# Kernel tuning notes

Hardware: AMD Instinct MI355X
Metric: run time of the kernel (lower is better)

The kernel has to match this reference:

```python
import jax, jax.numpy as jnp
import numpy as np

N, E, H, ED = 20000, 320000, 256, 64  # nodes, edges, hidden_dim, edge_feature_dim


def setup_inputs() -> dict:
    key = jax.random.key(0)
    ks = jax.random.split(key, 12)

    def init_w(k, shape, fan_in):
        return (jax.random.normal(k, shape, jnp.float32) / np.sqrt(fan_in)).astype(jnp.float32)

    h = jax.random.normal(ks[0], (N, H), jnp.float32)
    edge_indices = jax.random.randint(ks[1], (2, E), 0, N, jnp.int32)
    edge_attr = jax.random.normal(ks[2], (E, ED), jnp.float32)

    din = 2 * H + ED  # edge_network input: [h[row], h[col], edge_attr]
    W1 = init_w(ks[3], (H, din), din)
    b1 = jnp.zeros((H,), jnp.float32)
    W2 = init_w(ks[4], (H, H), H)
    b2 = jnp.zeros((H,), jnp.float32)
    # GRUCell params, gate order (r, z, n) as in torch
    W_ih = init_w(ks[5], (3 * H, H), H)
    b_ih = jnp.zeros((3 * H,), jnp.float32)
    W_hh = init_w(ks[6], (3 * H, H), H)
    b_hh = jnp.zeros((3 * H,), jnp.float32)

    return {"h": h, "edge_indices": edge_indices, "edge_attr": edge_attr,
            "W1": W1, "b1": b1, "W2": W2, "b2": b2,
            "W_ih": W_ih, "b_ih": b_ih, "W_hh": W_hh, "b_hh": b_hh}


def reference(h, edge_indices, edge_attr, W1, b1, W2, b2, W_ih, b_ih, W_hh, b_hh):
    row, col = edge_indices[0], edge_indices[1]
    # message: edge_network MLP on [h[row], h[col], edge_attr]
    edge_in = jnp.concatenate([h[row], h[col], edge_attr], axis=-1)  # [E, 2H+ED]
    msg = jax.nn.relu(edge_in @ W1.T + b1) @ W2.T + b2               # [E, H]
    # scatter_add aggregation by destination node (row)
    agg = jax.ops.segment_sum(msg, row, num_segments=h.shape[0])     # [N, H]
    # GRUCell update: input=agg, hidden=h
    gx = agg @ W_ih.T + b_ih
    gh = h @ W_hh.T + b_hh
    xr, xz, xn = jnp.split(gx, 3, axis=-1)
    hr, hz, hn = jnp.split(gh, 3, axis=-1)
    r = jax.nn.sigmoid(xr + hr)
    z = jax.nn.sigmoid(xz + hz)
    n = jnp.tanh(xn + r * hn)
    h_new = (1.0 - z) * n + z * h
    return h_new  # dropout p=0.0 -> identity
```

## Files before the change

kernel.cpp:

```cpp
#include <hip/hip_runtime.h>
#include <math.h>

#define NN 20000
#define NE 320000
#define HD 256
#define EDIM 64
#define DIN 576
#define ASTRIDE 264

typedef __attribute__((ext_vector_type(4))) _Float16 h4;
typedef __attribute__((ext_vector_type(8))) _Float16 h8;
typedef __attribute__((ext_vector_type(4))) float f32x4;

__device__ _Float16 g_W1cf[16 * 2 * 64 * 8];
__device__ _Float16 g_W12f[32 * 8 * 64 * 8];
__device__ _Float16 g_Wrzf[32 * 16 * 64 * 8];
__device__ _Float16 g_Wnxf[16 * 8 * 64 * 8];
__device__ _Float16 g_Wnhf[16 * 8 * 64 * 8];
__device__ float    g_Wib2[768];
__device__ _Float16 g_pre[(size_t)NN * 512];
__device__ _Float16 g_hf[(size_t)NN * 256];
__device__ _Float16 g_S16[(size_t)NN * 256];
__device__ _Float16 g_msg[(size_t)NE * 256];
__device__ int      g_rowptr[NN + 1];
__device__ int      g_cursor[NN];

__device__ __forceinline__ h4 f2h4(float4 v) {
  return (h4){(_Float16)v.x, (_Float16)v.y, (_Float16)v.z, (_Float16)v.w};
}
__device__ __forceinline__ h8 f2h8(float4 a, float4 b) {
  return (h8){(_Float16)a.x, (_Float16)a.y, (_Float16)a.z, (_Float16)a.w,
              (_Float16)b.x, (_Float16)b.y, (_Float16)b.z, (_Float16)b.w};
}

__global__ __launch_bounds__(256) void cvtfold_kernel(
    const float* __restrict__ W1, const float* __restrict__ W_hh,
    const float* __restrict__ W_ih, const float* __restrict__ W2,
    const float* __restrict__ b2)
{
  const int bid = blockIdx.x;
  if (bid < 768) {
    const int r = bid, c = threadIdx.x;
    const float* wr = W_ih + (size_t)r * HD;
    float acc = 0.f;
    for (int m = 0; m < HD; ++m) acc += wr[m] * W2[(size_t)m * HD + c];
    const int ks = c >> 5, lg = (c >> 3) & 3, j = c & 7;
    const int l = lg * 16 + (r & 15);
    if (r < 512) {
      const int cf = (r < 256) ? (r >> 4) : (16 + ((r - 256) >> 4));
      g_Wrzf[(size_t)((cf * 16 + ks) * 64 + l) * 8 + j] = (_Float16)acc;
    } else {
      const int cf = (r - 512) >> 4;
      g_Wnxf[(size_t)((cf * 8 + ks) * 64 + l) * 8 + j] = (_Float16)acc;
    }
    if (c == 0) {
      float a2 = 0.f;
      for (int m = 0; m < HD; ++m) a2 += wr[m] * b2[m];
      g_Wib2[r] = a2;
    }
    return;
  }
  const int idx = (bid - 768) * 256 + threadIdx.x;
  const int g = idx >> 6, l = idx & 63;
  const int r16 = l & 15, koff = (l >> 4) * 8;
  const float* src; _Float16* dst;
  if (g < 32) {
    const int cf = g >> 1, ks = g & 1;
    src = &W1[(size_t)(cf * 16 + r16) * DIN + 512 + ks * 32 + koff];
    dst = &g_W1cf[(size_t)(cf * 2 + ks) * 512 + l * 8];
  } else if (g < 288) {
    const int gg = g - 32, cf = gg >> 3, ks = gg & 7;
    src = (cf < 16) ? &W1[(size_t)(cf * 16 + r16) * DIN + ks * 32 + koff]
                    : &W1[(size_t)((cf - 16) * 16 + r16) * DIN + 256 + ks * 32 + koff];
    dst = &g_W12f[(size_t)(cf * 8 + ks) * 512 + l * 8];
  } else if (g < 544) {
    const int gg = g - 288, cf = gg >> 3, ks = 8 + (gg & 7);
    const int row = (cf < 16) ? cf * 16 + r16 : 256 + (cf - 16) * 16 + r16;
    src = &W_hh[(size_t)row * HD + (ks - 8) * 32 + koff];
    dst = &g_Wrzf[(size_t)(cf * 16 + ks) * 512 + l * 8];
  } else {
    const int gg = g - 544, cf = gg >> 3, ks = gg & 7;
    src = &W_hh[(size_t)(512 + cf * 16 + r16) * HD + ks * 32 + koff];
    dst = &g_Wnhf[(size_t)(cf * 8 + ks) * 512 + l * 8];
  }
#pragma unroll
  for (int j = 0; j < 8; ++j) dst[j] = (_Float16)src[j];
}

#define PSTR 264
__global__ __launch_bounds__(256, 4) void pre_kernel(const float* __restrict__ h,
                                                     const int* __restrict__ ei,
                                                     int* __restrict__ deg) {
  __shared__ _Float16 A[32 * PSTR];
  const int t = threadIdx.x, w = t >> 6, l = t & 63;
  const int l15 = l & 15, lg = l >> 4;
  const int nb = blockIdx.x * 32;

  {
    const int gid = blockIdx.x * 256 + t;
    atomicAdd(&deg[ei[gid]], 1);
    atomicAdd(&deg[ei[gid + NE / 2]], 1);
  }

  const int row = t >> 3, c8 = t & 7;
#pragma unroll
  for (int i = 0; i < 8; ++i) {
    const int col4 = c8 + i * 8;
    float4 v = ((const float4*)(h + (size_t)(nb + row) * HD))[col4];
    const h4 x = f2h4(v);
    *(h4*)&A[row * PSTR + col4 * 4] = x;
    *(h4*)&g_hf[(size_t)(nb + row) * 256 + col4 * 4] = x;
  }
  __syncthreads();

  f32x4 acc[2][8];
#pragma unroll
  for (int m = 0; m < 2; ++m)
#pragma unroll
    for (int n = 0; n < 8; ++n) acc[m][n] = (f32x4){0.f, 0.f, 0.f, 0.f};

  for (int ks = 0; ks < 8; ++ks) {
    h8 a[2];
#pragma unroll
    for (int m = 0; m < 2; ++m)
      a[m] = *(const h8*)&A[(m * 16 + l15) * PSTR + ks * 32 + lg * 8];
#pragma unroll
    for (int n = 0; n < 8; ++n) {
      const h8 b = *(const h8*)&g_W12f[(size_t)((w * 8 + n) * 8 + ks) * 512 + l * 8];
#pragma unroll
      for (int m = 0; m < 2; ++m)
        acc[m][n] = __builtin_amdgcn_mfma_f32_16x16x32_f16(a[m], b, acc[m][n], 0, 0, 0);
    }
  }

#pragma unroll
  for (int m = 0; m < 2; ++m)
#pragma unroll
    for (int n = 0; n < 8; ++n) {
      const int col = w * 128 + n * 16 + l15;
#pragma unroll
      for (int r = 0; r < 4; ++r)
        g_pre[(size_t)(nb + m * 16 + lg * 4 + r) * 512 + col] = (_Float16)acc[m][n][r];
    }
}

__global__ __launch_bounds__(512) void scan_kernel(const int* __restrict__ deg) {
  __shared__ int part[512];
  const int t = threadIdx.x;
  const int base = t * 40;
  int loc[40];
  int s = 0;
#pragma unroll
  for (int i = 0; i < 40; ++i) {
    const int idx = base + i;
    const int d = (idx < NN) ? deg[idx] : 0;
    loc[i] = s; s += d;
  }
  part[t] = s;
  __syncthreads();
  for (int off = 1; off < 512; off <<= 1) {
    const int v = (t >= off) ? part[t - off] : 0;
    __syncthreads();
    part[t] += v;
    __syncthreads();
  }
  const int pre = (t == 0) ? 0 : part[t - 1];
#pragma unroll
  for (int i = 0; i < 40; ++i) {
    const int idx = base + i;
    if (idx < NN) { const int v = pre + loc[i]; g_rowptr[idx] = v; g_cursor[idx] = v; }
  }
  if (t == 511) g_rowptr[NN] = part[511];
}

__global__ __launch_bounds__(256, 4) void msg_kernel(const float* __restrict__ eattr,
                                                     const int* __restrict__ ei) {
  __shared__ _Float16 T[64 * ASTRIDE];
  __shared__ int pL[64];
  const int t = threadIdx.x, w = t >> 6, l = t & 63;
  const int l15 = l & 15, lg = l >> 4;
  const int e0 = blockIdx.x * 64;

  if (t < 64) pL[t] = atomicAdd(&g_cursor[ei[e0 + t]], 1);

  h4 q2[16];
#pragma unroll
  for (int i = 0; i < 16; ++i) {
    const int srcn = ei[NE + e0 + w * 16 + i];
    q2[i] = *(const h4*)&g_pre[(size_t)srcn * 512 + 256 + l * 4];
  }

  f32x4 acc[4][4];
#pragma unroll
  for (int m = 0; m < 4; ++m)
#pragma unroll
    for (int n = 0; n < 4; ++n) acc[m][n] = (f32x4){0.f, 0.f, 0.f, 0.f};

#pragma unroll
  for (int ks = 0; ks < 2; ++ks) {
    h8 a[4], b[4];
#pragma unroll
    for (int m = 0; m < 4; ++m) {
      const float* ep = eattr + (size_t)(e0 + m * 16 + l15) * EDIM + ks * 32 + lg * 8;
      a[m] = f2h8(((const float4*)ep)[0], ((const float4*)ep)[1]);
    }
#pragma unroll
    for (int n = 0; n < 4; ++n)
      b[n] = *(const h8*)&g_W1cf[(size_t)((w * 4 + n) * 2 + ks) * 512 + l * 8];
#pragma unroll
    for (int m = 0; m < 4; ++m)
#pragma unroll
      for (int n = 0; n < 4; ++n)
        acc[m][n] = __builtin_amdgcn_mfma_f32_16x16x32_f16(a[m], b[n], acc[m][n], 0, 0, 0);
  }

#pragma unroll
  for (int m = 0; m < 4; ++m)
#pragma unroll
    for (int n = 0; n < 4; ++n)
#pragma unroll
      for (int r = 0; r < 4; ++r)
        T[(m * 16 + lg * 4 + r) * ASTRIDE + w * 64 + n * 16 + l15] = (_Float16)acc[m][n][r];
  __syncthreads();

#pragma unroll
  for (int i = 0; i < 16; ++i) {
    const int e = w * 16 + i;
    const h4 tt = *(const h4*)&T[e * ASTRIDE + l * 4];
    h4 o;
#pragma unroll
    for (int r = 0; r < 4; ++r)
      o[r] = (_Float16)((float)tt[r] + (float)q2[i][r]);
    *(h4*)&g_msg[(size_t)pL[e] * 256 + l * 4] = o;
  }
}

__global__ __launch_bounds__(256) void agg_kernel(const float* __restrict__ b1) {
  const int t = threadIdx.x, w = t >> 6, l = t & 63;
  const int n = blockIdx.x * 4 + w;
  const int start = g_rowptr[n];
  const int end = g_rowptr[n + 1];

  const h4 p1 = *(const h4*)&g_pre[(size_t)n * 512 + l * 4];
  const f32x4 b1v = *(const f32x4*)&b1[l * 4];
  f32x4 base;
#pragma unroll
  for (int r = 0; r < 4; ++r) base[r] = (float)p1[r] + b1v[r];

  f32x4 acc = (f32x4){0.f, 0.f, 0.f, 0.f};
  int p = start;
  for (; p + 4 <= end; p += 4) {
    h4 m[4];
#pragma unroll
    for (int k = 0; k < 4; ++k)
      m[k] = *(const h4*)&g_msg[(size_t)(p + k) * 256 + l * 4];
#pragma unroll
    for (int k = 0; k < 4; ++k)
#pragma unroll
      for (int r = 0; r < 4; ++r) {
        const float v = base[r] + (float)m[k][r];
        acc[r] += v > 0.f ? v : 0.f;
      }
  }
  for (; p < end; ++p) {
    const h4 m0 = *(const h4*)&g_msg[(size_t)p * 256 + l * 4];
#pragma unroll
    for (int r = 0; r < 4; ++r) {
      const float v = base[r] + (float)m0[r];
      acc[r] += v > 0.f ? v : 0.f;
    }
  }
  *(h4*)&g_S16[(size_t)n * 256 + l * 4] =
      (h4){(_Float16)acc[0], (_Float16)acc[1], (_Float16)acc[2], (_Float16)acc[3]};
}

__global__ __launch_bounds__(256, 2) void node_kernel(
    const float* __restrict__ b_ih, const float* __restrict__ b_hh,
    float* __restrict__ out)
{
  const int bid = blockIdx.x;
  const int cf = bid & 3, rng = bid >> 2;
  const int t = threadIdx.x, w = t >> 6, l = t & 63;
  const int l15 = l & 15, lg = l >> 4;
  const int nb = rng * 64;
  const int cf0 = cf * 4;
  int na = nb + w * 16 + l15; if (na >= NN) na = NN - 1;

  f32x4 ar[4], az[4], ax[4], ah[4];
#pragma unroll
  for (int n = 0; n < 4; ++n) {
    ar[n] = (f32x4){0.f, 0.f, 0.f, 0.f}; az[n] = (f32x4){0.f, 0.f, 0.f, 0.f};
    ax[n] = (f32x4){0.f, 0.f, 0.f, 0.f}; ah[n] = (f32x4){0.f, 0.f, 0.f, 0.f};
  }

  const _Float16* aS = &g_S16[(size_t)na * 256 + lg * 8];
  const _Float16* aH = &g_hf[(size_t)na * 256 + lg * 8];

#pragma unroll
  for (int ks = 0; ks < 8; ++ks) {
    const h8 a = *(const h8*)&aS[ks * 32];
    h8 br[4], bz[4], bn[4];
#pragma unroll
    for (int n = 0; n < 4; ++n) {
      br[n] = *(const h8*)&g_Wrzf[(size_t)(((cf0 + n) * 16 + ks) * 64 + l) * 8];
      bz[n] = *(const h8*)&g_Wrzf[(size_t)(((16 + cf0 + n) * 16 + ks) * 64 + l) * 8];
      bn[n] = *(const h8*)&g_Wnxf[(size_t)(((cf0 + n) * 8 + ks) * 64 + l) * 8];
    }
#pragma unroll
    for (int n = 0; n < 4; ++n) {
      ar[n] = __builtin_amdgcn_mfma_f32_16x16x32_f16(a, br[n], ar[n], 0, 0, 0);
      az[n] = __builtin_amdgcn_mfma_f32_16x16x32_f16(a, bz[n], az[n], 0, 0, 0);
      ax[n] = __builtin_amdgcn_mfma_f32_16x16x32_f16(a, bn[n], ax[n], 0, 0, 0);
    }
  }

#pragma unroll
  for (int ks = 0; ks < 8; ++ks) {
    const h8 a = *(const h8*)&aH[ks * 32];
    h8 br[4], bz[4], bn[4];
#pragma unroll
    for (int n = 0; n < 4; ++n) {
      br[n] = *(const h8*)&g_Wrzf[(size_t)(((cf0 + n) * 16 + 8 + ks) * 64 + l) * 8];
      bz[n] = *(const h8*)&g_Wrzf[(size_t)(((16 + cf0 + n) * 16 + 8 + ks) * 64 + l) * 8];
      bn[n] = *(const h8*)&g_Wnhf[(size_t)(((cf0 + n) * 8 + ks) * 64 + l) * 8];
    }
#pragma unroll
    for (int n = 0; n < 4; ++n) {
      ar[n] = __builtin_amdgcn_mfma_f32_16x16x32_f16(a, br[n], ar[n], 0, 0, 0);
      az[n] = __builtin_amdgcn_mfma_f32_16x16x32_f16(a, bz[n], az[n], 0, 0, 0);
      ah[n] = __builtin_amdgcn_mfma_f32_16x16x32_f16(a, bn[n], ah[n], 0, 0, 0);
    }
  }

#pragma unroll
  for (int r = 0; r < 4; ++r) {
    const int node = nb + w * 16 + lg * 4 + r;
    if (node >= NN) continue;
    const float df = (float)(g_rowptr[node + 1] - g_rowptr[node]);
#pragma unroll
    for (int n = 0; n < 4; ++n) {
      const int c = cf * 64 + n * 16 + l15;
      const float rg = 1.f / (1.f + __expf(-(ar[n][r] + df * g_Wib2[c] + b_ih[c] + b_hh[c])));
      const float zg = 1.f / (1.f + __expf(-(az[n][r] + df * g_Wib2[HD + c] + b_ih[HD + c] + b_hh[HD + c])));
      const float u  = ax[n][r] + df * g_Wib2[2 * HD + c] + b_ih[2 * HD + c]
                       + rg * (ah[n][r] + b_hh[2 * HD + c]);
      const float eu = __expf(2.f * fabsf(u));
      const float ng = copysignf(1.f - 2.f / (eu + 1.f), u);
      const float hv = (float)g_hf[(size_t)node * 256 + c];
      out[(size_t)node * HD + c] = (1.f - zg) * ng + zg * hv;
    }
  }
}

extern "C" void kernel_launch(void* const* d_in, const int* in_sizes, int n_in,
                              void* d_out, int out_size, void* d_ws, size_t ws_size,
                              hipStream_t stream)
{
  const float* h     = (const float*)d_in[0];
  const int*   ei    = (const int*)d_in[1];
  const float* eattr = (const float*)d_in[2];
  const float* W1    = (const float*)d_in[3];
  const float* b1    = (const float*)d_in[4];
  const float* W2    = (const float*)d_in[5];
  const float* b2    = (const float*)d_in[6];
  const float* W_ih  = (const float*)d_in[7];
  const float* b_ih  = (const float*)d_in[8];
  const float* W_hh  = (const float*)d_in[9];
  const float* b_hh  = (const float*)d_in[10];
  float* out = (float*)d_out;

  int* deg = (int*)d_ws;

  hipMemsetAsync(deg, 0, (size_t)NN * 4, stream);
  cvtfold_kernel<<<768 + 168, 256, 0, stream>>>(W1, W_hh, W_ih, W2, b2);
  pre_kernel<<<NN / 32, 256, 0, stream>>>(h, ei, deg);
  scan_kernel<<<1, 512, 0, stream>>>(deg);
  msg_kernel<<<NE / 64, 256, 0, stream>>>(eattr, ei);
  agg_kernel<<<NN / 4, 256, 0, stream>>>(b1);
  node_kernel<<<1252, 256, 0, stream>>>(b_ih, b_hh, out);
}
```

Measured before the change: 324.2 us.

## Sort edges by source node so message gathers of source projections are local

Adds source-degree counting and a second scan, plus a new permutation kernel that orders edges by source node. That kernel stores fp16 edge attributes in source order along with a link to each edge's destination-sorted slot. The message kernel then processes edges in source order, so the gathers of precomputed source projections hit repeated or nearby rows and reuse cache, and its scattered writes go to destination-ordered positions. The cost is an extra kernel launch, extra atomics, and an extra pass that writes and re-reads the edge attributes and index arrays.

```diff
diff --git a/kernel.cpp b/kernel.cpp
--- a/kernel.cpp
+++ b/kernel.cpp
@@ -21,9 +21,13 @@
 __device__ _Float16 g_pre[(size_t)NN * 512];
 __device__ _Float16 g_hf[(size_t)NN * 256];
 __device__ _Float16 g_S16[(size_t)NN * 256];
+__device__ _Float16 g_ea16[(size_t)NE * EDIM];
 __device__ _Float16 g_msg[(size_t)NE * 256];
 __device__ int      g_rowptr[NN + 1];
-__device__ int      g_cursor[NN];
+__device__ int      g_cursor_d[NN];
+__device__ int      g_cursor_s[NN];
+__device__ int      g_ssrc[NE];
+__device__ int      g_link[NE];
 
 __device__ __forceinline__ h4 f2h4(float4 v) {
   return (h4){(_Float16)v.x, (_Float16)v.y, (_Float16)v.z, (_Float16)v.w};
@@ -90,7 +94,8 @@
 #define PSTR 264
 __global__ __launch_bounds__(256, 4) void pre_kernel(const float* __restrict__ h,
                                                      const int* __restrict__ ei,
-                                                     int* __restrict__ deg) {
+                                                     int* __restrict__ deg_d,
+                                                     int* __restrict__ deg_s) {
   __shared__ _Float16 A[32 * PSTR];
   const int t = threadIdx.x, w = t >> 6, l = t & 63;
   const int l15 = l & 15, lg = l >> 4;
@@ -98,8 +103,10 @@
 
   {
     const int gid = blockIdx.x * 256 + t;
-    atomicAdd(&deg[ei[gid]], 1);
-    atomicAdd(&deg[ei[gid + NE / 2]], 1);
+    atomicAdd(&deg_d[ei[gid]], 1);
+    atomicAdd(&deg_d[ei[gid + NE / 2]], 1);
+    atomicAdd(&deg_s[ei[NE + gid]], 1);
+    atomicAdd(&deg_s[ei[NE + gid + NE / 2]], 1);
   }
 
   const int row = t >> 3, c8 = t & 7;
@@ -144,9 +151,12 @@
     }
 }
 
-__global__ __launch_bounds__(512) void scan_kernel(const int* __restrict__ deg) {
+__global__ __launch_bounds__(512) void scan_kernel(const int* __restrict__ deg_d,
+                                                   const int* __restrict__ deg_s) {
   __shared__ int part[512];
   const int t = threadIdx.x;
+  const int isD = blockIdx.x == 0;
+  const int* deg = isD ? deg_d : deg_s;
   const int base = t * 40;
   int loc[40];
   int s = 0;
@@ -168,27 +178,46 @@
 #pragma unroll
   for (int i = 0; i < 40; ++i) {
     const int idx = base + i;
-    if (idx < NN) { const int v = pre + loc[i]; g_rowptr[idx] = v; g_cursor[idx] = v; }
-  }
-  if (t == 511) g_rowptr[NN] = part[511];
-}
-
-__global__ __launch_bounds__(256, 4) void msg_kernel(const float* __restrict__ eattr,
-                                                     const int* __restrict__ ei) {
-  __shared__ _Float16 T[64 * ASTRIDE];
+    if (idx < NN) {
+      const int v = pre + loc[i];
+      if (isD) { g_rowptr[idx] = v; g_cursor_d[idx] = v; }
+      else     { g_cursor_s[idx] = v; }
+    }
+  }
+  if (isD && t == 511) g_rowptr[NN] = part[511];
+}
+
+__global__ __launch_bounds__(256) void perm_kernel(const float* __restrict__ eattr,
+                                                   const int* __restrict__ ei) {
   __shared__ int pL[64];
   const int t = threadIdx.x, w = t >> 6, l = t & 63;
+  const int e0 = blockIdx.x * 64;
+
+  if (t < 64) {
+    const int e = e0 + t;
+    const int dest = ei[e];
+    const int srcn = ei[NE + e];
+    const int ps = atomicAdd(&g_cursor_s[srcn], 1);
+    const int pd = atomicAdd(&g_cursor_d[dest], 1);
+    pL[t] = ps;
+    g_ssrc[ps] = srcn;
+    g_link[ps] = pd;
+  }
+  __syncthreads();
+
+#pragma unroll
+  for (int i = 0; i < 16; ++i) {
+    const int e = e0 + w * 16 + i;
+    const float v = eattr[(size_t)e * EDIM + l];
+    g_ea16[(size_t)pL[w * 16 + i] * EDIM + l] = (_Float16)v;
+  }
+}
+
+__global__ __launch_bounds__(256, 4) void msg_kernel() {
+  __shared__ _Float16 T[64 * ASTRIDE];
+  const int t = threadIdx.x, w = t >> 6, l = t & 63;
   const int l15 = l & 15, lg = l >> 4;
-  const int e0 = blockIdx.x * 64;
-
-  if (t < 64) pL[t] = atomicAdd(&g_cursor[ei[e0 + t]], 1);
-
-  h4 q2[16];
-#pragma unroll
-  for (int i = 0; i < 16; ++i) {
-    const int srcn = ei[NE + e0 + w * 16 + i];
-    q2[i] = *(const h4*)&g_pre[(size_t)srcn * 512 + 256 + l * 4];
-  }
+  const int p0 = blockIdx.x * 64;
 
   f32x4 acc[4][4];
 #pragma unroll
@@ -200,10 +229,8 @@
   for (int ks = 0; ks < 2; ++ks) {
     h8 a[4], b[4];
 #pragma unroll
-    for (int m = 0; m < 4; ++m) {
-      const float* ep = eattr + (size_t)(e0 + m * 16 + l15) * EDIM + ks * 32 + lg * 8;
-      a[m] = f2h8(((const float4*)ep)[0], ((const float4*)ep)[1]);
-    }
+    for (int m = 0; m < 4; ++m)
+      a[m] = *(const h8*)&g_ea16[(size_t)(p0 + m * 16 + l15) * EDIM + ks * 32 + lg * 8];
 #pragma unroll
     for (int n = 0; n < 4; ++n)
       b[n] = *(const h8*)&g_W1cf[(size_t)((w * 4 + n) * 2 + ks) * 512 + l * 8];
@@ -225,13 +252,16 @@
 
 #pragma unroll
   for (int i = 0; i < 16; ++i) {
-    const int e = w * 16 + i;
-    const h4 tt = *(const h4*)&T[e * ASTRIDE + l * 4];
+    const int p = p0 + w * 16 + i;
+    const int srcn = g_ssrc[p];
+    const int pd   = g_link[p];
+    const h4 tt = *(const h4*)&T[(w * 16 + i) * ASTRIDE + l * 4];
+    const h4 q2 = *(const h4*)&g_pre[(size_t)srcn * 512 + 256 + l * 4];
     h4 o;
 #pragma unroll
     for (int r = 0; r < 4; ++r)
-      o[r] = (_Float16)((float)tt[r] + (float)q2[i][r]);
-    *(h4*)&g_msg[(size_t)pL[e] * 256 + l * 4] = o;
+      o[r] = (_Float16)((float)tt[r] + (float)q2[r]);
+    *(h4*)&g_msg[(size_t)pd * 256 + l * 4] = o;
   }
 }
 
@@ -369,13 +399,15 @@
   const float* b_hh  = (const float*)d_in[10];
   float* out = (float*)d_out;
 
-  int* deg = (int*)d_ws;
-
-  hipMemsetAsync(deg, 0, (size_t)NN * 4, stream);
+  int* deg_d = (int*)d_ws;
+  int* deg_s = deg_d + NN;
+
+  hipMemsetAsync(d_ws, 0, (size_t)2 * NN * 4, stream);
   cvtfold_kernel<<<768 + 168, 256, 0, stream>>>(W1, W_hh, W_ih, W2, b2);
-  pre_kernel<<<NN / 32, 256, 0, stream>>>(h, ei, deg);
-  scan_kernel<<<1, 512, 0, stream>>>(deg);
-  msg_kernel<<<NE / 64, 256, 0, stream>>>(eattr, ei);
+  pre_kernel<<<NN / 32, 256, 0, stream>>>(h, ei, deg_d, deg_s);
+  scan_kernel<<<2, 512, 0, stream>>>(deg_d, deg_s);
+  perm_kernel<<<NE / 64, 256, 0, stream>>>(eattr, ei);
+  msg_kernel<<<NE / 64, 256, 0, stream>>>();
   agg_kernel<<<NN / 4, 256, 0, stream>>>(b1);
   node_kernel<<<1252, 256, 0, stream>>>(b_ih, b_hh, out);
 }
```

Measured after the change: 301.3 us. 7.1% less time.
